# Performance work log

Hardware: AMD Instinct MI355X
Metric: run time of the kernel (lower is better)

## Reference

```python
import jax, jax.numpy as jnp
import numpy as np

NUM_GROUPS = 32
EPS = 1e-6


def group_norm(x, gamma, beta):
    b, c, h, w = x.shape
    xg = x.reshape(b, NUM_GROUPS, c // NUM_GROUPS, h, w)
    mean = xg.mean(axis=(2, 3, 4), keepdims=True)
    var = xg.var(axis=(2, 3, 4), keepdims=True)
    xn = ((xg - mean) * jax.lax.rsqrt(var + EPS)).reshape(b, c, h, w)
    return xn * gamma[None, :, None, None] + beta[None, :, None, None]


def conv1x1(x, W, b):
    # x: [b,c,h,w], W: [c_out, c_in]
    return jnp.einsum('oi,bihw->bohw', W, x) + b[None, :, None, None]


def setup_inputs() -> dict:
    key = jax.random.key(0)
    ks = jax.random.split(key, 6)
    B, C, H, W = 4, 256, 64, 64
    s = 1.0 / np.sqrt(C)
    return {
        'x': jax.random.normal(ks[0], (B, C, H, W), jnp.float32),
        'gamma': jnp.ones((C,), jnp.float32),
        'beta': jnp.zeros((C,), jnp.float32),
        'Wq': jax.random.normal(ks[1], (C, C), jnp.float32) * s,
        'bq': jnp.zeros((C,), jnp.float32),
        'Wk': jax.random.normal(ks[2], (C, C), jnp.float32) * s,
        'bk': jnp.zeros((C,), jnp.float32),
        'Wv': jax.random.normal(ks[3], (C, C), jnp.float32) * s,
        'bv': jnp.zeros((C,), jnp.float32),
        'Wo': jax.random.normal(ks[4], (C, C), jnp.float32) * s,
        'bo': jnp.zeros((C,), jnp.float32),
    }


def reference(x, gamma, beta, Wq, bq, Wk, bk, Wv, bv, Wo, bo):
    attn_num = 1
    b, c, h, w = x.shape
    hn = group_norm(x, gamma, beta)
    q = conv1x1(hn, Wq, bq)
    k = conv1x1(hn, Wk, bk)
    v = conv1x1(hn, Wv, bv)
    ch = c // attn_num
    n = h * w
    q = q.reshape(b * attn_num, ch, n)
    k = k.reshape(b * attn_num, ch, n)
    v = v.reshape(b * attn_num, ch, n)
    # scores[g, i, j] = sum_c q[g,c,i] * k[g,c,j]; NOTE: scaled by full c, as in source
    scores = jnp.einsum('gci,gcj->gij', q, k) * (float(c) ** -0.5)
    attn = jax.nn.softmax(scores, axis=2)
    # h_[g,c,i] = sum_j v[g,c,j] * attn[g,i,j]
    out = jnp.einsum('gcj,gij->gci', v, attn).reshape(b, c, h, w)
    out = conv1x1(out, Wo, bo)
    return x + out
```

## Files before the change

kernel.cpp:

```cpp
#include <hip/hip_runtime.h>

typedef __attribute__((ext_vector_type(4))) float f32x4;
typedef __attribute__((ext_vector_type(8))) __bf16 bf16x8;

__device__ __forceinline__ unsigned short f2bf(float f) {
  unsigned int u = __float_as_uint(f);
  u += 0x7FFFu + ((u >> 16) & 1u);
  return (unsigned short)(u >> 16);
}
__device__ __forceinline__ float bf2f(unsigned short u) {
  return __uint_as_float(((unsigned int)u) << 16);
}
__device__ __forceinline__ float ex2(float x) {
  return __builtin_amdgcn_exp2f(x);
}

__device__ __forceinline__ void gload16(const void* g, void* l) {
  __builtin_amdgcn_global_load_lds(
      (const __attribute__((address_space(1))) void*)g,
      (__attribute__((address_space(3))) void*)l, 16, 0, 0);
}

#define QSCALE 0.09016844005555897f

__global__ __launch_bounds__(256)
void prep_weights(const float* __restrict__ wq, const float* __restrict__ wk,
                  const float* __restrict__ wv, const float* __restrict__ wo,
                  unsigned short* __restrict__ out) {
  int i = blockIdx.x * 256 + threadIdx.x;
  const float* src = (i < 65536) ? wq : (i < 131072) ? wk : (i < 196608) ? wv : wo;
  out[i] = f2bf(src[i & 65535]);
}

__global__ __launch_bounds__(512)
void groupnorm_split(const float* __restrict__ x, const float* __restrict__ gamma,
                     const float* __restrict__ beta, unsigned short* __restrict__ hnT) {
  const int blk = blockIdx.x;
  const int h = blk & 1, bg = blk >> 1;
  const int b = bg >> 5, g = bg & 31;
  const int tid = threadIdx.x;
  const float* xg = x + ((size_t)b * 256 + (size_t)g * 8) * 4096;
  const float* xo = xg + h * 2048;
  const float* xr = xg + (h ^ 1) * 2048;

  float v[8][4];
  float s = 0.f, ss = 0.f;
  #pragma unroll
  for (int c = 0; c < 8; ++c)
    #pragma unroll
    for (int s2 = 0; s2 < 4; ++s2) {
      float val = xo[c * 4096 + s2 * 512 + tid];
      v[c][s2] = val; s += val; ss += val * val;
    }
  #pragma unroll
  for (int c = 0; c < 8; ++c)
    #pragma unroll
    for (int s2 = 0; s2 < 4; ++s2) {
      float val = xr[c * 4096 + s2 * 512 + tid];
      s += val; ss += val * val;
    }
  __shared__ float rs[8], rss[8];
  for (int m = 1; m <= 32; m <<= 1) { s += __shfl_xor(s, m); ss += __shfl_xor(ss, m); }
  const int lane = tid & 63, wid = tid >> 6;
  if (lane == 0) { rs[wid] = s; rss[wid] = ss; }
  __syncthreads();
  s = 0.f; ss = 0.f;
  #pragma unroll
  for (int i = 0; i < 8; ++i) { s += rs[i]; ss += rss[i]; }
  const float mean = s * (1.f / 32768.f);
  const float var  = ss * (1.f / 32768.f) - mean * mean;
  const float rstd = rsqrtf(var + 1e-6f);

  float gk[8], bk2[8];
  #pragma unroll
  for (int c = 0; c < 8; ++c) {
    float ga = gamma[g * 8 + c] * rstd;
    gk[c]  = ga;
    bk2[c] = beta[g * 8 + c] - mean * ga;
  }
  unsigned short* outp = hnT + (size_t)b * 4096 * 256 + g * 8;
  #pragma unroll
  for (int s2 = 0; s2 < 4; ++s2) {
    const int n = h * 2048 + s2 * 512 + tid;
    union { unsigned short u[8]; uint4 q; } pk;
    #pragma unroll
    for (int c = 0; c < 8; ++c) pk.u[c] = f2bf(v[c][s2] * gk[c] + bk2[c]);
    *reinterpret_cast<uint4*>(outp + (size_t)n * 256) = pk.q;
  }
}

__global__ __launch_bounds__(256, 2)
void qkv_fused(const unsigned short* __restrict__ WB,
               const unsigned short* __restrict__ hnT,
               const float* __restrict__ bq, const float* __restrict__ bk,
               const float* __restrict__ bv,
               unsigned short* __restrict__ Qt, unsigned short* __restrict__ Kt,
               unsigned short* __restrict__ Vp) {
  __shared__ alignas(1024) unsigned char lds[32768];
  const int tid = threadIdx.x, lane = tid & 63, w = tid >> 6;
  const int hig = lane >> 4, l15 = lane & 15;
  const int z = blockIdx.y, nt = blockIdx.x;
  const int n0 = nt * 32;
  const size_t zoff = (size_t)z * 1048576;
  const unsigned short* hnB = hnT + zoff + (size_t)n0 * 256;

  #pragma unroll
  for (int p = 0; p < 4; ++p) {
    const int idx = p * 256 + tid;
    const int r = idx >> 5, sl = idx & 31;
    gload16(hnB + (size_t)r * 256 + ((sl ^ (r & 7)) << 3), lds + idx * 16);
  }

  const int qs = (lane & 3) ^ ((lane >> 3) & 3);
  const int ar = tid >> 2, asq = tid & 3;
  auto stageA = [&](int d, int s) {
    const unsigned short* base = WB + (s >> 3) * 32768 + (s & 7) * 32 + qs * 8;
    unsigned char* dst = lds + 16384 + d * 8192;
    gload16(base + (size_t)ar * 256,        dst + ar * 64 + asq * 16);
    gload16(base + (size_t)(ar + 64) * 256, dst + (ar + 64) * 64 + asq * 16);
  };

  const int aslot = hig ^ ((l15 >> 1) & 3);
  f32x4 acc[2][2] = {};

  stageA(0, 0);
  __syncthreads();

  for (int s = 0; s < 48; ++s) {
    const int d = s & 1;
    if (s + 1 < 48) stageA(d ^ 1, s + 1);
    const int kt = s & 7;
    bf16x8 af[2];
    #pragma unroll
    for (int mf = 0; mf < 2; ++mf)
      af[mf] = *reinterpret_cast<const bf16x8*>(
          lds + 16384 + d * 8192 + (w * 32 + mf * 16 + l15) * 64 + aslot * 16);
    #pragma unroll
    for (int nf = 0; nf < 2; ++nf) {
      const int rb = nf * 16 + l15;
      bf16x8 bfr = *reinterpret_cast<const bf16x8*>(
          lds + rb * 512 + (((kt * 4 + hig) ^ (rb & 7)) << 4));
      acc[0][nf] = __builtin_amdgcn_mfma_f32_16x16x32_bf16(af[0], bfr, acc[0][nf], 0, 0, 0);
      acc[1][nf] = __builtin_amdgcn_mfma_f32_16x16x32_bf16(af[1], bfr, acc[1][nf], 0, 0, 0);
    }
    if (kt == 7) {
      const int sel = s >> 3, wsel = sel >> 1, mh = sel & 1;
      #pragma unroll
      for (int mf = 0; mf < 2; ++mf) {
        const int gm0 = mh * 128 + w * 32 + mf * 16 + 4 * hig;
        #pragma unroll
        for (int nf = 0; nf < 2; ++nf) {
          const int n = n0 + nf * 16 + l15;
          if (wsel == 0) {
            ushort4 pk;
            pk.x = f2bf((acc[mf][nf][0] + bq[gm0])     * QSCALE);
            pk.y = f2bf((acc[mf][nf][1] + bq[gm0 + 1]) * QSCALE);
            pk.z = f2bf((acc[mf][nf][2] + bq[gm0 + 2]) * QSCALE);
            pk.w = f2bf((acc[mf][nf][3] + bq[gm0 + 3]) * QSCALE);
            *reinterpret_cast<ushort4*>(Qt + zoff + (size_t)n * 256 + gm0) = pk;
          } else if (wsel == 1) {
            ushort4 pk;
            pk.x = f2bf(acc[mf][nf][0] + bk[gm0]);
            pk.y = f2bf(acc[mf][nf][1] + bk[gm0 + 1]);
            pk.z = f2bf(acc[mf][nf][2] + bk[gm0 + 2]);
            pk.w = f2bf(acc[mf][nf][3] + bk[gm0 + 3]);
            *reinterpret_cast<ushort4*>(Kt + zoff + (size_t)n * 256 + gm0) = pk;
          } else {
            #pragma unroll
            for (int e = 0; e < 4; ++e)
              Vp[zoff + (size_t)(gm0 + e) * 4096 + n] = f2bf(acc[mf][nf][e] + bv[gm0 + e]);
          }
          acc[mf][nf] = f32x4{0.f, 0.f, 0.f, 0.f};
        }
      }
    }
    __syncthreads();
  }
}

__global__ __launch_bounds__(256, 2)
void flash_attn(const unsigned short* __restrict__ Qt,
                const unsigned short* __restrict__ Kt,
                const unsigned short* __restrict__ Vp,
                unsigned short* __restrict__ Opart, float* __restrict__ lpart) {
  __shared__ alignas(1024) unsigned char lds[81920];
  const int tid = threadIdx.x, lane = tid & 63, w = tid >> 6;
  const int hig = lane >> 4, l15 = lane & 15;
  const int bid = blockIdx.x;
  const int xcd = bid & 7, k = bid >> 3;
  const int combo = xcd * 2 + (k >> 5);
  const int jh = combo & 3, z = combo >> 2, qtb = k & 31;
  const size_t zoff = (size_t)z * 1048576;
  const unsigned short* Qz = Qt + zoff;
  const unsigned short* Kz = Kt + zoff;
  const unsigned short* Vz = Vp + zoff;
  const int q0 = qtb * 128 + w * 32;
  const int jb0 = jh * 1024;

  bf16x8 qfr[2][8];
  #pragma unroll
  for (int qf = 0; qf < 2; ++qf)
    #pragma unroll
    for (int ks = 0; ks < 8; ++ks)
      qfr[qf][ks] = *reinterpret_cast<const bf16x8*>(
          Qz + (size_t)(q0 + qf * 16 + l15) * 256 + ks * 32 + hig * 8);

  unsigned char* Pw = lds + 65536 + w * 4096;

  const unsigned short* pK[4];
  const unsigned short* pV[4];
  #pragma unroll
  for (int g = 0; g < 4; ++g) {
    const int jr = w * 8 + g * 2 + (lane >> 5);
    pK[g] = Kz + (size_t)(jb0 + jr) * 256 + (((lane & 31) ^ (jr & 7)) << 3);
    const int rloc = lane >> 3;
    const int sraw = (lane & 7) ^ rloc;
    const int cV = 2 * (w * 32 + g * 8 + rloc) + (sraw >> 2);
    pV[g] = Vz + (size_t)cV * 4096 + jb0 + (sraw & 3) * 8;
  }

  auto stage = [&](int d, int t) {
    unsigned char* Kd = lds + d * 16384 + w * 4096;
    unsigned char* Vd = lds + 32768 + d * 16384 + w * 4096;
    #pragma unroll
    for (int g = 0; g < 4; ++g) gload16(pK[g] + (size_t)t * 8192, Kd + g * 1024);
    #pragma unroll
    for (int g = 0; g < 4; ++g) gload16(pV[g] + (size_t)t * 32, Vd + g * 1024);
  };

  f32x4 o0[16] = {}, o1[16] = {};
  float l0 = 0.f, l1 = 0.f;

  stage(0, 0);
  for (int t = 0; t < 32; ++t) {
    asm volatile("s_waitcnt vmcnt(0)" ::: "memory");
    __builtin_amdgcn_s_barrier();
    __builtin_amdgcn_sched_barrier(0);
    const int cur = t & 1;
    if (t + 1 < 32) stage(cur ^ 1, t + 1);

    const unsigned char* Kb = lds + cur * 16384;
    const unsigned char* Vb = lds + 32768 + cur * 16384;

    f32x4 sA[2][2] = {};
    __builtin_amdgcn_s_setprio(1);
    #pragma unroll
    for (int ks = 0; ks < 8; ++ks) {
      #pragma unroll
      for (int jf = 0; jf < 2; ++jf) {
        const int jl = jf * 16 + l15;
        bf16x8 kf = *reinterpret_cast<const bf16x8*>(
            Kb + jl * 512 + (((4 * ks + hig) ^ (jl & 7)) << 4));
        sA[jf][0] = __builtin_amdgcn_mfma_f32_16x16x32_bf16(kf, qfr[0][ks], sA[jf][0], 0, 0, 0);
        sA[jf][1] = __builtin_amdgcn_mfma_f32_16x16x32_bf16(kf, qfr[1][ks], sA[jf][1], 0, 0, 0);
      }
    }
    __builtin_amdgcn_s_setprio(0);

    #pragma unroll
    for (int jf = 0; jf < 2; ++jf) {
      const int so = (((2 * jf + (hig >> 1)) ^ (l15 & 7)) << 4) + ((hig & 1) << 3);
      {
        float p0 = ex2(sA[jf][0][0]), p1 = ex2(sA[jf][0][1]);
        float p2 = ex2(sA[jf][0][2]), p3 = ex2(sA[jf][0][3]);
        l0 += (p0 + p1) + (p2 + p3);
        union { __bf16 b[4]; uint2 u; } pk;
        pk.b[0] = (__bf16)p0; pk.b[1] = (__bf16)p1;
        pk.b[2] = (__bf16)p2; pk.b[3] = (__bf16)p3;
        *reinterpret_cast<uint2*>(Pw + l15 * 128 + so) = pk.u;
      }
      {
        float p0 = ex2(sA[jf][1][0]), p1 = ex2(sA[jf][1][1]);
        float p2 = ex2(sA[jf][1][2]), p3 = ex2(sA[jf][1][3]);
        l1 += (p0 + p1) + (p2 + p3);
        union { __bf16 b[4]; uint2 u; } pk;
        pk.b[0] = (__bf16)p0; pk.b[1] = (__bf16)p1;
        pk.b[2] = (__bf16)p2; pk.b[3] = (__bf16)p3;
        *reinterpret_cast<uint2*>(Pw + (16 + l15) * 128 + so) = pk.u;
      }
    }

    const int pso = (hig ^ (l15 & 7)) << 4;
    bf16x8 pa0 = *reinterpret_cast<const bf16x8*>(Pw + l15 * 128 + pso);
    bf16x8 pa1 = *reinterpret_cast<const bf16x8*>(Pw + (16 + l15) * 128 + pso);
    const int vslot = ((l15 & 1) * 4 + hig) ^ (l15 >> 1);
    __builtin_amdgcn_s_setprio(1);
    #pragma unroll
    for (int nf = 0; nf < 16; ++nf) {
      bf16x8 vb = *reinterpret_cast<const bf16x8*>(
          Vb + (8 * nf + (l15 >> 1)) * 128 + (vslot << 4));
      o0[nf] = __builtin_amdgcn_mfma_f32_16x16x32_bf16(pa0, vb, o0[nf], 0, 0, 0);
      o1[nf] = __builtin_amdgcn_mfma_f32_16x16x32_bf16(pa1, vb, o1[nf], 0, 0, 0);
    }
    __builtin_amdgcn_s_setprio(0);
  }

  l0 += __shfl_xor(l0, 16); l0 += __shfl_xor(l0, 32);
  l1 += __shfl_xor(l1, 16); l1 += __shfl_xor(l1, 32);

  unsigned short* Ob = Opart + ((size_t)(jh * 4 + z) * 4096 + q0) * 256;
  #pragma unroll
  for (int qf = 0; qf < 2; ++qf)
    #pragma unroll
    for (int nf = 0; nf < 16; ++nf)
      #pragma unroll
      for (int e = 0; e < 4; ++e) {
        const int row = qf * 16 + 4 * hig + e;
        Ob[(size_t)row * 256 + nf * 16 + l15] = f2bf((qf == 0) ? o0[nf][e] : o1[nf][e]);
      }
  if (hig == 0) {
    const size_t mb = (size_t)(jh * 4 + z) * 4096 + q0;
    lpart[mb + l15] = l0;  lpart[mb + 16 + l15] = l1;
  }
}

__global__ __launch_bounds__(256)
void flash_merge(const unsigned short* __restrict__ Opart,
                 const float* __restrict__ lpart, unsigned short* __restrict__ Ht) {
  const int t = threadIdx.x;
  const int r = blockIdx.x * 4 + (t >> 6);
  const int c = (t & 63) * 4;
  const int z = r >> 12, n = r & 4095;
  float lsum = 0.f;
  #pragma unroll
  for (int h = 0; h < 4; ++h) lsum += lpart[(h * 4 + z) * 4096 + n];
  const float inv = 1.f / lsum;
  float acc[4] = {};
  #pragma unroll
  for (int h = 0; h < 4; ++h) {
    ushort4 v = *reinterpret_cast<const ushort4*>(
        Opart + ((size_t)((h * 4 + z) * 4096 + n)) * 256 + c);
    acc[0] += bf2f(v.x); acc[1] += bf2f(v.y);
    acc[2] += bf2f(v.z); acc[3] += bf2f(v.w);
  }
  ushort4 pk;
  pk.x = f2bf(acc[0] * inv); pk.y = f2bf(acc[1] * inv);
  pk.z = f2bf(acc[2] * inv); pk.w = f2bf(acc[3] * inv);
  *reinterpret_cast<ushort4*>(Ht + (size_t)r * 256 + c) = pk;
}

__global__ __launch_bounds__(256)
void gemm_out(const unsigned short* __restrict__ A,
              const unsigned short* __restrict__ B, long bStrideZ,
              float* __restrict__ Out, long oStrideZ,
              const float* __restrict__ bias,
              const float* __restrict__ resid, long rStrideZ,
              int M, int N, int K) {
  __shared__ alignas(1024) unsigned char lds[32768];
  const int tid  = threadIdx.x;
  const int lane = tid & 63;
  const int hi   = lane >> 4;
  const int l15  = lane & 15;
  const int wid  = tid >> 6;
  const int wm = wid >> 1, wn = wid & 1;
  const int z  = blockIdx.z;
  const int m0 = blockIdx.y * 128;
  const int n0 = blockIdx.x * 128;
  const unsigned short* Az = A;
  const unsigned short* Bz = B + (size_t)z * bStrideZ;

  const int c0 = wid * 2, c1 = wid * 2 + 1;
  const int rr = lane >> 2;
  const int qs = (lane & 3) ^ ((lane >> 3) & 3);
  const unsigned short* pa0 = Az + (size_t)(m0 + c0 * 16 + rr) * K + qs * 8;
  const unsigned short* pa1 = Az + (size_t)(m0 + c1 * 16 + rr) * K + qs * 8;
  const unsigned short* pb0 = Bz + (size_t)(n0 + c0 * 16 + rr) * K + qs * 8;
  const unsigned short* pb1 = Bz + (size_t)(n0 + c1 * 16 + rr) * K + qs * 8;
  unsigned char* lA0 = lds + c0 * 1024;
  unsigned char* lA1 = lds + c1 * 1024;
  unsigned char* lB0 = lds + 8192 + c0 * 1024;
  unsigned char* lB1 = lds + 8192 + c1 * 1024;

  const int slot = hi ^ ((l15 >> 1) & 3);
  int roffA[4], roffB[4];
  #pragma unroll
  for (int t = 0; t < 4; ++t) {
    roffA[t] = (wm * 64 + t * 16 + l15) * 64 + slot * 16;
    roffB[t] = 8192 + (wn * 64 + t * 16 + l15) * 64 + slot * 16;
  }

  f32x4 acc[4][4] = {};

  const int nk = K >> 5;
  gload16(pa0, lA0); gload16(pa1, lA1);
  gload16(pb0, lB0); gload16(pb1, lB1);
  __syncthreads();

  int cur = 0;
  for (int kt = 0; kt < nk; ++kt) {
    if (kt + 1 < nk) {
      const size_t ko = (size_t)(kt + 1) * 32;
      const int bo = (cur ^ 1) * 16384;
      gload16(pa0 + ko, lA0 + bo); gload16(pa1 + ko, lA1 + bo);
      gload16(pb0 + ko, lB0 + bo); gload16(pb1 + ko, lB1 + bo);
    }
    const unsigned char* base = lds + cur * 16384;
    bf16x8 af[4], bfr[4];
    #pragma unroll
    for (int t = 0; t < 4; ++t) {
      af[t]  = *reinterpret_cast<const bf16x8*>(base + roffA[t]);
      bfr[t] = *reinterpret_cast<const bf16x8*>(base + roffB[t]);
    }
    #pragma unroll
    for (int mt = 0; mt < 4; ++mt)
      #pragma unroll
      for (int nt = 0; nt < 4; ++nt)
        acc[mt][nt] = __builtin_amdgcn_mfma_f32_16x16x32_bf16(af[mt], bfr[nt], acc[mt][nt], 0, 0, 0);
    __syncthreads();
    cur ^= 1;
  }

  const int gmb = m0 + wm * 64;
  const int gnb = n0 + wn * 64;
  float* O = Out + (size_t)z * oStrideZ;
  const float* R = resid + (size_t)z * rStrideZ;
  #pragma unroll
  for (int mt = 0; mt < 4; ++mt) {
    const int gm0 = gmb + mt * 16 + 4 * hi;
    #pragma unroll
    for (int nt = 0; nt < 4; ++nt) {
      const int gn = gnb + nt * 16 + l15;
      #pragma unroll
      for (int e = 0; e < 4; ++e) {
        size_t idx = (size_t)(gm0 + e) * N + gn;
        O[idx] = acc[mt][nt][e] + bias[gm0 + e] + R[idx];
      }
    }
  }
}

__global__ void ws_too_small(float* out, float v) {
  if (threadIdx.x == 0 && blockIdx.x == 0) out[0] = v;
}

extern "C" void kernel_launch(void* const* d_in, const int* in_sizes, int n_in,
                              void* d_out, int out_size, void* d_ws, size_t ws_size,
                              hipStream_t stream) {
  const float* x     = (const float*)d_in[0];
  const float* gamma = (const float*)d_in[1];
  const float* beta  = (const float*)d_in[2];
  const float* Wq    = (const float*)d_in[3];
  const float* bq    = (const float*)d_in[4];
  const float* Wk    = (const float*)d_in[5];
  const float* bk    = (const float*)d_in[6];
  const float* Wv    = (const float*)d_in[7];
  const float* bv    = (const float*)d_in[8];
  const float* Wo    = (const float*)d_in[9];
  const float* bo    = (const float*)d_in[10];
  float* out = (float*)d_out;

  unsigned char* ws = (unsigned char*)d_ws;
  unsigned short* WB    = (unsigned short*)(ws);
  unsigned short* hnT   = (unsigned short*)(ws + 524288);
  float*          lpart = (float*)(ws + 524288);
  unsigned short* Qt    = (unsigned short*)(ws + 8912896);
  unsigned short* Kt    = (unsigned short*)(ws + 17301504);
  unsigned short* V     = (unsigned short*)(ws + 25690112);
  unsigned short* Ht    = (unsigned short*)(ws + 34078720);
  unsigned short* Opart = (unsigned short*)(ws + 42467328);

  if (ws_size < 76283904) {
    hipMemsetAsync(d_out, 0, (size_t)out_size * 4, stream);
    ws_too_small<<<1, 64, 0, stream>>>(out, (float)ws_size);
    return;
  }

  prep_weights<<<1024, 256, 0, stream>>>(Wq, Wk, Wv, Wo, WB);
  groupnorm_split<<<256, 512, 0, stream>>>(x, gamma, beta, hnT);

  qkv_fused<<<dim3(128, 4), 256, 0, stream>>>(WB, hnT, bq, bk, bv, Qt, Kt, V);

  flash_attn<<<512, 256, 0, stream>>>(Qt, Kt, V, Opart, lpart);
  flash_merge<<<4096, 256, 0, stream>>>(Opart, lpart, Ht);

  gemm_out<<<dim3(32, 2, 4), 256, 0, stream>>>(
      WB + 196608, Ht, 1048576, out, 1048576, bo, x, 1048576, 256, 4096, 256);
}
```

Measured before the change: 137.1 us.

## Fuse flash-attention split merge into output projection GEMM

Removes the separate flash_merge kernel and has gemm_out read the four partial attention outputs directly. It sums them while staging B tiles into LDS, and applies the 1/l normalization in the epilogue. This saves a kernel launch and a round trip of the merged Ht buffer through global memory. In exchange, the B-tile loads become synchronous register loads with bf16 arithmetic instead of async global_load_lds, and each gemm_out block now reads four times as much B data, since both m-tile blocks redo the merge.

```diff
diff --git a/kernel.cpp b/kernel.cpp
--- a/kernel.cpp
+++ b/kernel.cpp
@@ -315,33 +315,9 @@
 }
 
 __global__ __launch_bounds__(256)
-void flash_merge(const unsigned short* __restrict__ Opart,
-                 const float* __restrict__ lpart, unsigned short* __restrict__ Ht) {
-  const int t = threadIdx.x;
-  const int r = blockIdx.x * 4 + (t >> 6);
-  const int c = (t & 63) * 4;
-  const int z = r >> 12, n = r & 4095;
-  float lsum = 0.f;
-  #pragma unroll
-  for (int h = 0; h < 4; ++h) lsum += lpart[(h * 4 + z) * 4096 + n];
-  const float inv = 1.f / lsum;
-  float acc[4] = {};
-  #pragma unroll
-  for (int h = 0; h < 4; ++h) {
-    ushort4 v = *reinterpret_cast<const ushort4*>(
-        Opart + ((size_t)((h * 4 + z) * 4096 + n)) * 256 + c);
-    acc[0] += bf2f(v.x); acc[1] += bf2f(v.y);
-    acc[2] += bf2f(v.z); acc[3] += bf2f(v.w);
-  }
-  ushort4 pk;
-  pk.x = f2bf(acc[0] * inv); pk.y = f2bf(acc[1] * inv);
-  pk.z = f2bf(acc[2] * inv); pk.w = f2bf(acc[3] * inv);
-  *reinterpret_cast<ushort4*>(Ht + (size_t)r * 256 + c) = pk;
-}
-
-__global__ __launch_bounds__(256)
 void gemm_out(const unsigned short* __restrict__ A,
-              const unsigned short* __restrict__ B, long bStrideZ,
+              const unsigned short* __restrict__ Opart,
+              const float* __restrict__ lpart,
               float* __restrict__ Out, long oStrideZ,
               const float* __restrict__ bias,
               const float* __restrict__ resid, long rStrideZ,
@@ -356,20 +332,29 @@
   const int z  = blockIdx.z;
   const int m0 = blockIdx.y * 128;
   const int n0 = blockIdx.x * 128;
-  const unsigned short* Az = A;
-  const unsigned short* Bz = B + (size_t)z * bStrideZ;
+  const size_t CH = 4194304;
 
   const int c0 = wid * 2, c1 = wid * 2 + 1;
   const int rr = lane >> 2;
   const int qs = (lane & 3) ^ ((lane >> 3) & 3);
-  const unsigned short* pa0 = Az + (size_t)(m0 + c0 * 16 + rr) * K + qs * 8;
-  const unsigned short* pa1 = Az + (size_t)(m0 + c1 * 16 + rr) * K + qs * 8;
-  const unsigned short* pb0 = Bz + (size_t)(n0 + c0 * 16 + rr) * K + qs * 8;
-  const unsigned short* pb1 = Bz + (size_t)(n0 + c1 * 16 + rr) * K + qs * 8;
+  const unsigned short* pa0 = A + (size_t)(m0 + c0 * 16 + rr) * K + qs * 8;
+  const unsigned short* pa1 = A + (size_t)(m0 + c1 * 16 + rr) * K + qs * 8;
+  const unsigned short* pb0 = Opart + (size_t)(z * 4096 + n0 + c0 * 16 + rr) * 256 + qs * 8;
+  const unsigned short* pb1 = Opart + (size_t)(z * 4096 + n0 + c1 * 16 + rr) * 256 + qs * 8;
   unsigned char* lA0 = lds + c0 * 1024;
   unsigned char* lA1 = lds + c1 * 1024;
-  unsigned char* lB0 = lds + 8192 + c0 * 1024;
-  unsigned char* lB1 = lds + 8192 + c1 * 1024;
+
+  auto sum4 = [&](const unsigned short* p) -> uint4 {
+    union U { uint4 v; unsigned short u[8]; } a, b, c, d, r;
+    a.v = *reinterpret_cast<const uint4*>(p);
+    b.v = *reinterpret_cast<const uint4*>(p + CH);
+    c.v = *reinterpret_cast<const uint4*>(p + 2 * CH);
+    d.v = *reinterpret_cast<const uint4*>(p + 3 * CH);
+    #pragma unroll
+    for (int i = 0; i < 8; ++i)
+      r.u[i] = f2bf((bf2f(a.u[i]) + bf2f(b.u[i])) + (bf2f(c.u[i]) + bf2f(d.u[i])));
+    return r.v;
+  };
 
   const int slot = hi ^ ((l15 >> 1) & 3);
   int roffA[4], roffB[4];
@@ -383,16 +368,19 @@
 
   const int nk = K >> 5;
   gload16(pa0, lA0); gload16(pa1, lA1);
-  gload16(pb0, lB0); gload16(pb1, lB1);
+  *reinterpret_cast<uint4*>(lds + 8192 + c0 * 1024 + lane * 16) = sum4(pb0);
+  *reinterpret_cast<uint4*>(lds + 8192 + c1 * 1024 + lane * 16) = sum4(pb1);
   __syncthreads();
 
   int cur = 0;
   for (int kt = 0; kt < nk; ++kt) {
+    const int bo = (cur ^ 1) * 16384;
+    uint4 sb0, sb1;
     if (kt + 1 < nk) {
       const size_t ko = (size_t)(kt + 1) * 32;
-      const int bo = (cur ^ 1) * 16384;
       gload16(pa0 + ko, lA0 + bo); gload16(pa1 + ko, lA1 + bo);
-      gload16(pb0 + ko, lB0 + bo); gload16(pb1 + ko, lB1 + bo);
+      sb0 = sum4(pb0 + ko);
+      sb1 = sum4(pb1 + ko);
     }
     const unsigned char* base = lds + cur * 16384;
     bf16x8 af[4], bfr[4];
@@ -406,6 +394,10 @@
       #pragma unroll
       for (int nt = 0; nt < 4; ++nt)
         acc[mt][nt] = __builtin_amdgcn_mfma_f32_16x16x32_bf16(af[mt], bfr[nt], acc[mt][nt], 0, 0, 0);
+    if (kt + 1 < nk) {
+      *reinterpret_cast<uint4*>(lds + bo + 8192 + c0 * 1024 + lane * 16) = sb0;
+      *reinterpret_cast<uint4*>(lds + bo + 8192 + c1 * 1024 + lane * 16) = sb1;
+    }
     __syncthreads();
     cur ^= 1;
   }
@@ -414,6 +406,14 @@
   const int gnb = n0 + wn * 64;
   float* O = Out + (size_t)z * oStrideZ;
   const float* R = resid + (size_t)z * rStrideZ;
+  float invl[4];
+  #pragma unroll
+  for (int nt = 0; nt < 4; ++nt) {
+    const int gn = gnb + nt * 16 + l15;
+    float ls = (lpart[(size_t)z * 4096 + gn]            + lpart[(size_t)(4 + z) * 4096 + gn]) +
+               (lpart[(size_t)(8 + z) * 4096 + gn]      + lpart[(size_t)(12 + z) * 4096 + gn]);
+    invl[nt] = 1.f / ls;
+  }
   #pragma unroll
   for (int mt = 0; mt < 4; ++mt) {
     const int gm0 = gmb + mt * 16 + 4 * hi;
@@ -423,7 +423,7 @@
       #pragma unroll
       for (int e = 0; e < 4; ++e) {
         size_t idx = (size_t)(gm0 + e) * N + gn;
-        O[idx] = acc[mt][nt][e] + bias[gm0 + e] + R[idx];
+        O[idx] = acc[mt][nt][e] * invl[nt] + bias[gm0 + e] + R[idx];
       }
     }
   }
@@ -456,7 +456,6 @@
   unsigned short* Qt    = (unsigned short*)(ws + 8912896);
   unsigned short* Kt    = (unsigned short*)(ws + 17301504);
   unsigned short* V     = (unsigned short*)(ws + 25690112);
-  unsigned short* Ht    = (unsigned short*)(ws + 34078720);
   unsigned short* Opart = (unsigned short*)(ws + 42467328);
 
   if (ws_size < 76283904) {
@@ -471,8 +470,7 @@
   qkv_fused<<<dim3(128, 4), 256, 0, stream>>>(WB, hnT, bq, bk, bv, Qt, Kt, V);
 
   flash_attn<<<512, 256, 0, stream>>>(Qt, Kt, V, Opart, lpart);
-  flash_merge<<<4096, 256, 0, stream>>>(Opart, lpart, Ht);
 
   gemm_out<<<dim3(32, 2, 4), 256, 0, stream>>>(
-      WB + 196608, Ht, 1048576, out, 1048576, bo, x, 1048576, 256, 4096, 256);
-}
+      WB + 196608, Opart, lpart, out, 1048576, bo, x, 1048576, 256, 4096, 256);
+}
```

New measurement: 135.8 us. About the same (-1.0%).
